# Kernel tuning notes

Hardware: AMD Instinct MI355X
Metric: run time of the kernel (lower is better)

## Reference

```python
import jax, jax.numpy as jnp
import numpy as np

B, Q, K, H, DQ, DK, DV = 8, 256, 256, 256, 256, 256, 256


def setup_inputs() -> dict:
    key = jax.random.key(0)
    k1, k2, k3, k4, k5, k6, k7 = jax.random.split(key, 7)
    queries = jax.random.normal(k1, (B, Q, DQ), dtype=jnp.float32)
    keys = jax.random.normal(k2, (B, K, DK), dtype=jnp.float32)
    values = jax.random.normal(k3, (B, K, DV), dtype=jnp.float32)
    valid_lens = jax.random.randint(k4, (B,), 1, K + 1)
    # learned params (torch Linear without bias); stored as (in, out)
    s = 1.0 / np.sqrt(H)
    W_q = jax.random.uniform(k5, (DQ, H), minval=-s, maxval=s, dtype=jnp.float32)
    W_k = jax.random.uniform(k6, (DK, H), minval=-s, maxval=s, dtype=jnp.float32)
    w_v = jax.random.uniform(k7, (H,), minval=-s, maxval=s, dtype=jnp.float32)
    return {"queries": queries, "keys": keys, "values": values,
            "valid_lens": valid_lens, "W_q": W_q, "W_k": W_k, "w_v": w_v}


def reference(queries, keys, values, valid_lens, W_q, W_k, w_v):
    q = queries @ W_q                      # (B, Q, H)
    k = keys @ W_k                         # (B, K, H)
    # broadcast add + tanh -> (B, Q, K, H), then linear score -> (B, Q, K)
    features = jnp.tanh(q[:, :, None, :] + k[:, None, :, :])
    scores = jnp.einsum('bqkh,h->bqk', features, w_v)
    mask = jnp.arange(K)[None, None, :] >= valid_lens[:, None, None]  # (B,1,K)
    scores = jnp.where(mask, -1000000.0, scores)
    attn = jax.nn.softmax(scores, axis=-1)  # (B, Q, K)
    return jnp.einsum('bqk,bkd->bqd', attn, values)  # (B, Q, DV)
```

## Files before the change

kernel.cpp:

```cpp
#include <hip/hip_runtime.h>
#include <hip/hip_bf16.h>

#define LOG2E 1.4426950408889634f
#define C2    (2.0f * LOG2E)

static __device__ __forceinline__ float fast_exp2(float x) {
#if __has_builtin(__builtin_amdgcn_exp2f)
  return __builtin_amdgcn_exp2f(x);
#else
  return exp2f(x);
#endif
}
static __device__ __forceinline__ float fast_rcp(float x) {
#if __has_builtin(__builtin_amdgcn_rcpf)
  return __builtin_amdgcn_rcpf(x);
#else
  return 1.0f / x;
#endif
}

typedef short bf16x8 __attribute__((ext_vector_type(8)));
typedef float f32x4  __attribute__((ext_vector_type(4)));

static __device__ __forceinline__ short f2bf(float x) {
  unsigned u = __float_as_uint(x);
  u += 0x7fff + ((u >> 16) & 1);
  return (short)(u >> 16);
}

__global__ __launch_bounds__(256, 4) void proj_kernel(
    const float* __restrict__ queries, const float* __restrict__ keys,
    const float* __restrict__ W_q,     const float* __restrict__ W_k,
    const int*   __restrict__ vlen,
    float* __restrict__ qs, float* __restrict__ ks_p)
{
  const int bz = blockIdx.z;
  const float* X = bz ? keys : queries;
  const float* W = bz ? W_k  : W_q;
  const int n0 = blockIdx.x * 32;
  const int m0 = blockIdx.y * 64;

  if (bz == 1) {
    const int vl = vlen[m0 >> 8];
    if ((m0 & 255) >= vl) return;
  }

  const int t = threadIdx.x;
  const int l = t & 63;
  const int w = t >> 6;

  __shared__ short Wp[8 * 2 * 64 * 8];

  {
    const int nl = t & 31, ko = t >> 5;
#pragma unroll
    for (int rep = 0; rep < 4; ++rep) {
      const int koct = ko + rep * 8;
      const int kc  = koct >> 2;
      const int grp = koct & 3;
      const int nt  = nl >> 4;
      const int ln  = grp * 16 + (nl & 15);
      short w8[8];
#pragma unroll
      for (int jj = 0; jj < 8; ++jj)
        w8[jj] = f2bf(W[(size_t)(koct * 8 + jj) * 256 + n0 + nl]);
      *(bf16x8*)&Wp[((kc * 2 + nt) * 64 + ln) * 8] = *(bf16x8*)w8;
    }
  }
  __syncthreads();

  const int mb   = m0 + w * 16;
  const int row  = mb + (l & 15);
  const int kofs = (l >> 4) * 8;

  f32x4 acc0 = {0.f, 0.f, 0.f, 0.f};
  f32x4 acc1 = {0.f, 0.f, 0.f, 0.f};
#pragma unroll
  for (int kc = 0; kc < 8; ++kc) {
    float4 a0 = *(const float4*)&X[(size_t)row * 256 + kc * 32 + kofs];
    float4 a1 = *(const float4*)&X[(size_t)row * 256 + kc * 32 + kofs + 4];
    bf16x8 af;
    af[0] = f2bf(a0.x); af[1] = f2bf(a0.y); af[2] = f2bf(a0.z); af[3] = f2bf(a0.w);
    af[4] = f2bf(a1.x); af[5] = f2bf(a1.y); af[6] = f2bf(a1.z); af[7] = f2bf(a1.w);
    bf16x8 b0 = *(bf16x8*)&Wp[((kc * 2 + 0) * 64 + l) * 8];
    bf16x8 b1 = *(bf16x8*)&Wp[((kc * 2 + 1) * 64 + l) * 8];
    acc0 = __builtin_amdgcn_mfma_f32_16x16x32_bf16(af, b0, acc0, 0, 0, 0);
    acc1 = __builtin_amdgcn_mfma_f32_16x16x32_bf16(af, b1, acc1, 0, 0, 0);
  }

  const int c = l & 15;
#pragma unroll
  for (int nt = 0; nt < 2; ++nt) {
    const f32x4 acc = nt ? acc1 : acc0;
    const int n = n0 + nt * 16 + c;
#pragma unroll
    for (int j = 0; j < 4; ++j) {
      const int rj = (l >> 4) * 4 + j;
      const float o = fast_exp2(acc[j] * C2);
      if (bz == 0) {
        qs[(size_t)(mb + rj) * 256 + n] = o;
      } else {
        const int b  = mb >> 8;
        const int kl = (mb & 255) + rj;
        ks_p[((size_t)(b * 64 + (n >> 2)) * 256 + kl) * 4 + (n & 3)] = o;
      }
    }
  }
}

#define SC_PAIR_Q(qv, qi, ca, cb)                                          \
  {                                                                        \
    float t0 = fmaf(qv.ca, kv[j].ca, 1.f);                                 \
    float t1 = fmaf(qv.cb, kv[j].cb, 1.f);                                 \
    float num = fmaf(wv.ca, t1, wv.cb * t0);                               \
    sc[j][qi] = fmaf(num, fast_rcp(t0 * t1), sc[j][qi]);                   \
  }

template <int NJ>
__device__ __forceinline__ void score_loop(
    const float* __restrict__ kp,
    const float* __restrict__ qp,
    const float* __restrict__ wvp, int h4b, float (&sc)[4][4])
{
#pragma unroll 2
  for (int h4 = h4b; h4 < h4b + 8; ++h4) {
    float4 kv[NJ];
#pragma unroll
    for (int j = 0; j < NJ; ++j)
      kv[j] = *(const float4*)(kp + h4 * 1024 + j * 256);
    float4 qv0 = *(const float4*)(qp + 0 * 256 + h4 * 4);
    float4 qv1 = *(const float4*)(qp + 1 * 256 + h4 * 4);
    float4 qv2 = *(const float4*)(qp + 2 * 256 + h4 * 4);
    float4 qv3 = *(const float4*)(qp + 3 * 256 + h4 * 4);
    float4 wv  = *(const float4*)(wvp + h4 * 4);
#pragma unroll
    for (int j = 0; j < NJ; ++j) {
      SC_PAIR_Q(qv0, 0, x, y); SC_PAIR_Q(qv1, 1, x, y);
      SC_PAIR_Q(qv2, 2, x, y); SC_PAIR_Q(qv3, 3, x, y);
      SC_PAIR_Q(qv0, 0, z, w); SC_PAIR_Q(qv1, 1, z, w);
      SC_PAIR_Q(qv2, 2, z, w); SC_PAIR_Q(qv3, 3, z, w);
    }
  }
}

__global__ __launch_bounds__(512, 4) void attn_kernel(
    const float* __restrict__ qs, const float* __restrict__ ks_p,
    const float* __restrict__ values, const int* __restrict__ vlen,
    const float* __restrict__ w_v, float* __restrict__ out)
{
  const int t    = threadIdx.x;
  const int lane = t & 63;
  const int w    = t >> 6;
  const int bx   = blockIdx.x;

  int njv[8];
#pragma unroll
  for (int i = 0; i < 8; ++i) njv[i] = (vlen[i] + 63) >> 6;
  unsigned packed = 0, rem = 0xFFu;
#pragma unroll
  for (int r = 0; r < 8; ++r) {
    int best = -1, bi = 0;
#pragma unroll
    for (int i = 0; i < 8; ++i) {
      if (rem & (1u << i)) {
        int key = njv[i] * 8 + (7 - i);
        if (key > best) { best = key; bi = i; }
      }
    }
    packed |= (unsigned)bi << (3 * r);
    rem &= ~(1u << bi);
  }
  const int jpair = bx & 3;
  const int hi    = (bx >> 8) & 1;
  const int sel   = hi ? (7 - jpair) : jpair;
  const int b     = (int)((packed >> (3 * sel)) & 7u);
  const int q0    = ((bx >> 2) & 63) * 4;

  __shared__ __align__(16) float sbuf[8192];
  __shared__ __align__(16) float p2[256 * 4];
  __shared__ float rsum_lds[4];

  const int vl = vlen[b];
  const int nj = njv[0] * 0 + ((vl + 63) >> 6);

  float s0 = w_v[lane] + w_v[lane + 64] + w_v[lane + 128] + w_v[lane + 192];
#pragma unroll
  for (int off = 32; off; off >>= 1) s0 += __shfl_xor(s0, off);
  const float Wsum = s0;

  const float* qp = qs + (size_t)(b * 256 + q0) * 256;
  const float* kp = ks_p + (size_t)b * 65536 + lane * 4;
  const int h4b = w * 8;

  float sc[4][4] = {};
  switch (nj) {
    case 1:  score_loop<1>(kp, qp, w_v, h4b, sc); break;
    case 2:  score_loop<2>(kp, qp, w_v, h4b, sc); break;
    case 3:  score_loop<3>(kp, qp, w_v, h4b, sc); break;
    default: score_loop<4>(kp, qp, w_v, h4b, sc); break;
  }

#pragma unroll
  for (int j = 0; j < 4; ++j)
    *(float4*)&sbuf[((w * 4 + j) * 64 + lane) * 4] =
        make_float4(sc[j][0], sc[j][1], sc[j][2], sc[j][3]);
  __syncthreads();

  if (w < 4) {
    const int q = w;
    float scores[4];
    float mx = -3.4e38f;
#pragma unroll 4
    for (int j = 0; j < nj; ++j) {
      float s = 0.f;
#pragma unroll
      for (int ww = 0; ww < 8; ++ww)
        s += sbuf[((ww * 4 + j) * 64 + lane) * 4 + q];
      float v = Wsum - 2.f * s;
      if (j * 64 + lane >= vl) v = -1000000.0f;
      scores[j] = v;
      mx = fmaxf(mx, v);
    }
#pragma unroll
    for (int off = 32; off; off >>= 1) mx = fmaxf(mx, __shfl_xor(mx, off));
    float sum = 0.f;
#pragma unroll 4
    for (int j = 0; j < nj; ++j) {
      float p = fast_exp2((scores[j] - mx) * LOG2E);
      p2[(j * 64 + lane) * 4 + q] = p;
      sum += p;
    }
#pragma unroll
    for (int off = 32; off; off >>= 1) sum += __shfl_xor(sum, off);
    if (lane == 0) rsum_lds[q] = sum;
  }
  __syncthreads();

  float4 acc[4];
#pragma unroll
  for (int q = 0; q < 4; ++q) acc[q] = make_float4(0.f, 0.f, 0.f, 0.f);
  const float* Vb = values + (size_t)b * 65536 + lane * 4;
  if (w < vl) {
    float4 v0 = *(const float4*)(Vb + (size_t)w * 256);
    float4 v1 = (w + 8 < vl) ? *(const float4*)(Vb + (size_t)(w + 8) * 256)
                             : make_float4(0.f, 0.f, 0.f, 0.f);
    for (int k = w; k < vl; k += 8) {
      float4 vn = (k + 16 < vl)
                      ? *(const float4*)(Vb + (size_t)(k + 16) * 256)
                      : make_float4(0.f, 0.f, 0.f, 0.f);
      float4 pk = *(const float4*)&p2[k * 4];
      acc[0].x = fmaf(pk.x, v0.x, acc[0].x);
      acc[0].y = fmaf(pk.x, v0.y, acc[0].y);
      acc[0].z = fmaf(pk.x, v0.z, acc[0].z);
      acc[0].w = fmaf(pk.x, v0.w, acc[0].w);
      acc[1].x = fmaf(pk.y, v0.x, acc[1].x);
      acc[1].y = fmaf(pk.y, v0.y, acc[1].y);
      acc[1].z = fmaf(pk.y, v0.z, acc[1].z);
      acc[1].w = fmaf(pk.y, v0.w, acc[1].w);
      acc[2].x = fmaf(pk.z, v0.x, acc[2].x);
      acc[2].y = fmaf(pk.z, v0.y, acc[2].y);
      acc[2].z = fmaf(pk.z, v0.z, acc[2].z);
      acc[2].w = fmaf(pk.z, v0.w, acc[2].w);
      acc[3].x = fmaf(pk.w, v0.x, acc[3].x);
      acc[3].y = fmaf(pk.w, v0.y, acc[3].y);
      acc[3].z = fmaf(pk.w, v0.z, acc[3].z);
      acc[3].w = fmaf(pk.w, v0.w, acc[3].w);
      v0 = v1; v1 = vn;
    }
  }
#pragma unroll
  for (int q = 0; q < 4; ++q)
    *(float4*)&sbuf[(w * 4 + q) * 256 + lane * 4] = acc[q];
  __syncthreads();

#pragma unroll
  for (int rep = 0; rep < 2; ++rep) {
    int o = t + rep * 512;
    int q = o >> 8, d = o & 255;
    float s = 0.f;
#pragma unroll
    for (int ww = 0; ww < 8; ++ww) s += sbuf[(ww * 4 + q) * 256 + d];
    out[(size_t)(b * 256 + q0 + q) * 256 + d] = s * fast_rcp(rsum_lds[q]);
  }
}

extern "C" void kernel_launch(void* const* d_in, const int* in_sizes, int n_in,
                              void* d_out, int out_size, void* d_ws, size_t ws_size,
                              hipStream_t stream) {
  const float* queries = (const float*)d_in[0];
  const float* keys    = (const float*)d_in[1];
  const float* values  = (const float*)d_in[2];
  const int*   vlenp   = (const int*)d_in[3];
  const float* W_q     = (const float*)d_in[4];
  const float* W_k     = (const float*)d_in[5];
  const float* w_v     = (const float*)d_in[6];
  float* out = (float*)d_out;

  float* qs   = (float*)d_ws;
  float* ks_p = qs + 2048 * 256;

  dim3 pgrid(8, 32, 2);
  proj_kernel<<<pgrid, 256, 0, stream>>>(queries, keys, W_q, W_k, vlenp, qs, ks_p);
  attn_kernel<<<512, 512, 0, stream>>>(qs, ks_p, values, vlenp, w_v, out);
}
```

Measured before the change: 33.38 us.

## Split projection K-reduction across two wave groups and merge tanh terms four at a time

The projection kernel now runs 512 threads per block. Two groups of four waves each handle half of the K=256 reduction, and the partial accumulators are combined through shared memory before the exp epilogue. Separately, the score loop folds four tanh-ratio terms into a single reciprocal instead of two, which cuts the number of transcendental ops. The price is an extra LDS round-trip and barrier in projection, plus a higher risk of precision loss or overflow from multiplying four (1+e^x) factors together.

```diff
diff --git a/kernel.cpp b/kernel.cpp
--- a/kernel.cpp
+++ b/kernel.cpp
@@ -28,7 +28,7 @@
   return (short)(u >> 16);
 }
 
-__global__ __launch_bounds__(256, 4) void proj_kernel(
+__global__ __launch_bounds__(512, 4) void proj_kernel(
     const float* __restrict__ queries, const float* __restrict__ keys,
     const float* __restrict__ W_q,     const float* __restrict__ W_k,
     const int*   __restrict__ vlen,
@@ -50,12 +50,13 @@
   const int w = t >> 6;
 
   __shared__ short Wp[8 * 2 * 64 * 8];
+  __shared__ __align__(16) float pacc[4 * 64 * 8];
 
   {
     const int nl = t & 31, ko = t >> 5;
 #pragma unroll
-    for (int rep = 0; rep < 4; ++rep) {
-      const int koct = ko + rep * 8;
+    for (int rep = 0; rep < 2; ++rep) {
+      const int koct = ko + rep * 16;
       const int kc  = koct >> 2;
       const int grp = koct & 3;
       const int nt  = nl >> 4;
@@ -69,14 +70,17 @@
   }
   __syncthreads();
 
-  const int mb   = m0 + w * 16;
+  const int g2   = w >> 2;
+  const int wq   = w & 3;
+  const int mb   = m0 + wq * 16;
   const int row  = mb + (l & 15);
   const int kofs = (l >> 4) * 8;
 
   f32x4 acc0 = {0.f, 0.f, 0.f, 0.f};
   f32x4 acc1 = {0.f, 0.f, 0.f, 0.f};
 #pragma unroll
-  for (int kc = 0; kc < 8; ++kc) {
+  for (int kk = 0; kk < 4; ++kk) {
+    const int kc = g2 * 4 + kk;
     float4 a0 = *(const float4*)&X[(size_t)row * 256 + kc * 32 + kofs];
     float4 a1 = *(const float4*)&X[(size_t)row * 256 + kc * 32 + kofs + 4];
     bf16x8 af;
@@ -88,32 +92,51 @@
     acc1 = __builtin_amdgcn_mfma_f32_16x16x32_bf16(af, b1, acc1, 0, 0, 0);
   }
 
-  const int c = l & 15;
-#pragma unroll
-  for (int nt = 0; nt < 2; ++nt) {
-    const f32x4 acc = nt ? acc1 : acc0;
-    const int n = n0 + nt * 16 + c;
-#pragma unroll
-    for (int j = 0; j < 4; ++j) {
-      const int rj = (l >> 4) * 4 + j;
-      const float o = fast_exp2(acc[j] * C2);
-      if (bz == 0) {
-        qs[(size_t)(mb + rj) * 256 + n] = o;
-      } else {
-        const int b  = mb >> 8;
-        const int kl = (mb & 255) + rj;
-        ks_p[((size_t)(b * 64 + (n >> 2)) * 256 + kl) * 4 + (n & 3)] = o;
+  if (g2 == 1) {
+    *(float4*)&pacc[(wq * 64 + l) * 8 + 0] =
+        make_float4(acc0[0], acc0[1], acc0[2], acc0[3]);
+    *(float4*)&pacc[(wq * 64 + l) * 8 + 4] =
+        make_float4(acc1[0], acc1[1], acc1[2], acc1[3]);
+  }
+  __syncthreads();
+  if (g2 == 0) {
+    float4 p0 = *(const float4*)&pacc[(wq * 64 + l) * 8 + 0];
+    float4 p1 = *(const float4*)&pacc[(wq * 64 + l) * 8 + 4];
+    acc0[0] += p0.x; acc0[1] += p0.y; acc0[2] += p0.z; acc0[3] += p0.w;
+    acc1[0] += p1.x; acc1[1] += p1.y; acc1[2] += p1.z; acc1[3] += p1.w;
+
+    const int c = l & 15;
+#pragma unroll
+    for (int nt = 0; nt < 2; ++nt) {
+      const f32x4 acc = nt ? acc1 : acc0;
+      const int n = n0 + nt * 16 + c;
+#pragma unroll
+      for (int j = 0; j < 4; ++j) {
+        const int rj = (l >> 4) * 4 + j;
+        const float o = fast_exp2(acc[j] * C2);
+        if (bz == 0) {
+          qs[(size_t)(mb + rj) * 256 + n] = o;
+        } else {
+          const int b  = mb >> 8;
+          const int kl = (mb & 255) + rj;
+          ks_p[((size_t)(b * 64 + (n >> 2)) * 256 + kl) * 4 + (n & 3)] = o;
+        }
       }
     }
   }
 }
 
-#define SC_PAIR_Q(qv, qi, ca, cb)                                          \
+#define SC_QUAD_Q(qv, qi)                                                  \
   {                                                                        \
-    float t0 = fmaf(qv.ca, kv[j].ca, 1.f);                                 \
-    float t1 = fmaf(qv.cb, kv[j].cb, 1.f);                                 \
-    float num = fmaf(wv.ca, t1, wv.cb * t0);                               \
-    sc[j][qi] = fmaf(num, fast_rcp(t0 * t1), sc[j][qi]);                   \
+    float t0 = fmaf(qv.x, kv[j].x, 1.f);                                   \
+    float t1 = fmaf(qv.y, kv[j].y, 1.f);                                   \
+    float t2 = fmaf(qv.z, kv[j].z, 1.f);                                   \
+    float t3 = fmaf(qv.w, kv[j].w, 1.f);                                   \
+    float t01 = t0 * t1, t23 = t2 * t3;                                    \
+    float n01 = fmaf(wv.x, t1, wv.y * t0);                                 \
+    float n23 = fmaf(wv.z, t3, wv.w * t2);                                 \
+    float num = fmaf(n01, t23, n23 * t01);                                 \
+    sc[j][qi] = fmaf(num, fast_rcp(t01 * t23), sc[j][qi]);                 \
   }
 
 template <int NJ>
@@ -135,10 +158,8 @@
     float4 wv  = *(const float4*)(wvp + h4 * 4);
 #pragma unroll
     for (int j = 0; j < NJ; ++j) {
-      SC_PAIR_Q(qv0, 0, x, y); SC_PAIR_Q(qv1, 1, x, y);
-      SC_PAIR_Q(qv2, 2, x, y); SC_PAIR_Q(qv3, 3, x, y);
-      SC_PAIR_Q(qv0, 0, z, w); SC_PAIR_Q(qv1, 1, z, w);
-      SC_PAIR_Q(qv2, 2, z, w); SC_PAIR_Q(qv3, 3, z, w);
+      SC_QUAD_Q(qv0, 0); SC_QUAD_Q(qv1, 1);
+      SC_QUAD_Q(qv2, 2); SC_QUAD_Q(qv3, 3);
     }
   }
 }
@@ -181,7 +202,7 @@
   __shared__ float rsum_lds[4];
 
   const int vl = vlen[b];
-  const int nj = njv[0] * 0 + ((vl + 63) >> 6);
+  const int nj = (vl + 63) >> 6;
 
   float s0 = w_v[lane] + w_v[lane + 64] + w_v[lane + 128] + w_v[lane + 192];
 #pragma unroll
@@ -300,6 +321,6 @@
   float* ks_p = qs + 2048 * 256;
 
   dim3 pgrid(8, 32, 2);
-  proj_kernel<<<pgrid, 256, 0, stream>>>(queries, keys, W_q, W_k, vlenp, qs, ks_p);
+  proj_kernel<<<pgrid, 512, 0, stream>>>(queries, keys, W_q, W_k, vlenp, qs, ks_p);
   attn_kernel<<<512, 512, 0, stream>>>(qs, ks_p, values, vlenp, w_v, out);
 }
```

Result: no change. 33.54 us (+0.5%).
